# Kernel tuning notes

Measured on AMD Instinct MI355X. Metric: run time of the kernel, lower is better.

## Reference

```python
import jax, jax.numpy as jnp
import numpy as np

H, C = 2, 32  # heads, out_channels per head
NEG_SLOPE = 0.2


def gatv2_layer(h, src, dst, ea, W, b, We, att, bias, N):
    # shared lin_l = lin_r (share_weights=True)
    z = (h @ W + b).reshape(N, H, C)                      # [N,H,C]
    e = (ea @ We).reshape(-1, H, C)                        # [E',H,C]
    s = jax.nn.leaky_relu(z[dst] + z[src] + e, NEG_SLOPE)  # [E',H,C]
    alpha = jnp.einsum('ehc,hc->eh', s, att)               # [E',H]
    # segment softmax over destination neighborhoods
    m = jax.ops.segment_max(alpha, dst, num_segments=N)
    m = jnp.where(jnp.isfinite(m), m, 0.0)
    ex = jnp.exp(alpha - m[dst])
    denom = jax.ops.segment_sum(ex, dst, num_segments=N)
    a = ex / (denom[dst] + 1e-16)                          # [E',H]
    msg = (z[src] * a[:, :, None]).reshape(-1, H * C)      # [E',H*C]
    out = jax.ops.segment_sum(msg, dst, num_segments=N) + bias
    return out                                             # [N,H*C]


def setup_inputs() -> dict:
    key = jax.random.key(0)
    ks = jax.random.split(key, 16)
    N, E = 50000, 800000
    inp = {
        'x': jax.random.normal(ks[0], (N, 2), jnp.float32),
        'edge_index': jax.random.randint(ks[1], (2, E), 0, N, jnp.int64 if jax.config.jax_enable_x64 else jnp.int32).astype(jnp.int32),
        'edge_attr': jax.random.uniform(ks[2], (E, 2), jnp.float32),
        'dest_index': 123,
        'W0': jax.random.normal(ks[3], (2, 64), jnp.float32) * 0.5,
        'b0': jnp.zeros((64,), jnp.float32),
        'We0': jax.random.normal(ks[4], (2, 64), jnp.float32) * 0.5,
        'att0': jax.random.normal(ks[5], (H, C), jnp.float32) * 0.5,
        'bias0': jnp.zeros((64,), jnp.float32),
        'W1': jax.random.normal(ks[6], (64, 64), jnp.float32) * 0.125,
        'b1': jnp.zeros((64,), jnp.float32),
        'We1': jax.random.normal(ks[7], (2, 64), jnp.float32) * 0.5,
        'att1': jax.random.normal(ks[8], (H, C), jnp.float32) * 0.5,
        'bias1': jnp.zeros((64,), jnp.float32),
        'Wm1': jax.random.normal(ks[9], (194, 32), jnp.float32) * 0.07,
        'bm1': jnp.zeros((32,), jnp.float32),
        'Wm2': jax.random.normal(ks[10], (32, 1), jnp.float32) * 0.17,
        'bm2': jnp.zeros((1,), jnp.float32),
    }
    return inp


def reference(x, edge_index, edge_attr, dest_index,
              W0, b0, We0, att0, bias0,
              W1, b1, We1, att1, bias1,
              Wm1, bm1, Wm2, bm2):
    N = x.shape[0]
    # add self loops (fill_value='mean' for edge_attr)
    loops = jnp.arange(N, dtype=edge_index.dtype)
    src = jnp.concatenate([edge_index[0], loops])
    dst = jnp.concatenate([edge_index[1], loops])
    ea_sl = jnp.concatenate(
        [edge_attr, jnp.broadcast_to(edge_attr.mean(axis=0), (N, edge_attr.shape[1]))], axis=0)

    h = x
    h = jax.nn.elu(gatv2_layer(h, src, dst, ea_sl, W0, b0, We0, att0, bias0, N))
    h = jax.nn.elu(gatv2_layer(h, src, dst, ea_sl, W1, b1, We1, att1, bias1, N))

    goal = h[dest_index]                                   # [64]
    src_emb = h[edge_index[0]]                             # [E,64]
    dst_emb = h[edge_index[1]]                             # [E,64]
    goal_rep = jnp.broadcast_to(goal, (edge_index.shape[1], goal.shape[0]))
    edge_in = jnp.concatenate([src_emb, dst_emb, goal_rep, edge_attr], axis=-1)  # [E,194]
    hmlp = jax.nn.relu(edge_in @ Wm1 + bm1)
    logits = (hmlp @ Wm2 + bm2).squeeze(-1)                # [E]
    return logits
```

## Files before the change

### kernel.cpp

```cpp
#include <hip/hip_runtime.h>
#include <hip/hip_bf16.h>
#include <hip/hip_fp16.h>
#include <math.h>


typedef __attribute__((ext_vector_type(8))) short short8;
typedef __attribute__((ext_vector_type(4))) float f32x4;

#define BSH 7
#define CAP 4096
#define CH 4096

template <int IMM>
__device__ __forceinline__ float swz(float x) {
    return __int_as_float(__builtin_amdgcn_ds_swizzle(__float_as_int(x), IMM));
}

template <int CTRL>
__device__ __forceinline__ float dpp_add(float p) {
    int t = __builtin_amdgcn_update_dpp(0, __float_as_int(p), CTRL, 0xF, 0xF, true);
    return p + __int_as_float(t);
}

__device__ __forceinline__ short2 bsplit(float x) {
    unsigned u = __float_as_uint(x);
    short hi = (short)(u >> 16);
    float hif = __uint_as_float(u & 0xFFFF0000u);
    short lo = (short)(__float_as_uint(x - hif) >> 16);
    return make_short2(hi, lo);
}

__global__ __launch_bounds__(512) void setup_kernel(const float* __restrict__ W1,
                                                    const float* __restrict__ Wm1,
                                                    short* __restrict__ BfW1,
                                                    short* __restrict__ BfWm,
                                                    int* __restrict__ bucket_cursor,
                                                    float* __restrict__ easum, int nbuck) {
    if (blockIdx.x == 2) {
        for (int i = threadIdx.x; i < nbuck; i += 512) bucket_cursor[i] = i * CAP;
        if (threadIdx.x < 2) easum[threadIdx.x] = 0.f;
        return;
    }
    int snt = threadIdx.x >> 6;
    int lane = threadIdx.x & 63;
    int s = snt >> 2, nt = snt & 3;
    int col = nt * 16 + (lane & 15);
    short* Bf = blockIdx.x == 0 ? BfW1 : BfWm;
#pragma unroll
    for (int j = 0; j < 8; ++j) {
        int k = s * 32 + (lane >> 4) * 8 + j;
        float v;
        if (blockIdx.x == 0) {
            v = W1[k * 64 + col];
        } else {
            v = (col < 32) ? Wm1[k * 32 + col] : Wm1[(64 + k) * 32 + (col - 32)];
        }
        short2 t = bsplit(v);
        Bf[(snt * 2 + 0) * 512 + lane * 8 + j] = t.x;
        Bf[(snt * 2 + 1) * 512 + lane * 8 + j] = t.y;
    }
}

__global__ __launch_bounds__(256) void phaseA_kernel(const int* __restrict__ ei,
                                                     const float2* __restrict__ ea,
                                                     int* __restrict__ bucket_cursor,
                                                     float* __restrict__ easum,
                                                     float4* __restrict__ staged,
                                                     int E, int nbuck) {
    extern __shared__ int sm[];
    int* lcnt = sm;
    int* lbase = sm + nbuck;
    __shared__ float r0[4], r1[4];
    int tid = threadIdx.x;
    for (int i = tid; i < nbuck; i += 256) lcnt[i] = 0;
    __syncthreads();
    int base = blockIdx.x * CH;
    int end = min(base + CH, E);
    for (int i = base + tid; i < end; i += 256) {
        int d = ei[E + i];
        atomicAdd(&lcnt[d >> BSH], 1);
    }
    __syncthreads();
    for (int i = tid; i < nbuck; i += 256) {
        int c = lcnt[i];
        lbase[i] = c ? atomicAdd(&bucket_cursor[i], c) : 0;
        lcnt[i] = 0;
    }
    __syncthreads();
    float s0 = 0.f, s1 = 0.f;
    for (int i = base + tid; i < end; i += 256) {
        int s = ei[i], d = ei[E + i];
        float2 v = ea[i];
        s0 += v.x; s1 += v.y;
        int b = d >> BSH;
        int pos = lbase[b] + atomicAdd(&lcnt[b], 1);
        staged[pos] = make_float4(__int_as_float(s), v.x, v.y, __int_as_float(d));
    }
#pragma unroll
    for (int o = 32; o >= 1; o >>= 1) {
        s0 += __shfl_xor(s0, o);
        s1 += __shfl_xor(s1, o);
    }
    int wave = tid >> 6;
    if ((tid & 63) == 0) { r0[wave] = s0; r1[wave] = s1; }
    __syncthreads();
    if (tid == 0) {
        atomicAdd(&easum[0], r0[0] + r0[1] + r0[2] + r0[3]);
        atomicAdd(&easum[1], r1[0] + r1[1] + r1[2] + r1[3]);
    }
}

__global__ __launch_bounds__(512) void phaseB_mega(
    const float4* __restrict__ staged, const int* __restrict__ bucket_cursor,
    const float* __restrict__ easum, const float2* __restrict__ x,
    const float* __restrict__ W0, const float* __restrict__ b0,
    const float* __restrict__ We, const float* __restrict__ att,
    const float* __restrict__ bias, const short* __restrict__ Bf,
    const float* __restrict__ b1,
    int* __restrict__ row_ptr, float4* __restrict__ recs,
    __half* __restrict__ z16, int N, int E, int nbuck) {
    __shared__ int cnt128[128];
    __shared__ int offs[128];
    __shared__ int psum[512];
    __shared__ float acc6[128][6];
    __shared__ float h0s[128 * 64];
    int b = blockIdx.x;
    int n0g = b << BSH;
    int tid = threadIdx.x;
    int local = 0;
    for (int j = tid; j < b; j += 512) local += bucket_cursor[j] - j * CAP;
    psum[tid] = local;
    if (tid < 128) cnt128[tid] = 0;
    for (int i = tid; i < 128 * 6; i += 512) ((float*)acc6)[i] = 0.f;
    __syncthreads();
    for (int st = 256; st > 0; st >>= 1) {
        if (tid < st) psum[tid] += psum[tid + st];
        __syncthreads();
    }
    int bbase = psum[0] + 128 * b;
    int sbeg = b * CAP;
    int send = bucket_cursor[b];
    for (int i = sbeg + tid; i < send; i += 512) {
        int d = __float_as_int(staged[i].w);
        atomicAdd(&cnt128[d - n0g], 1);
    }
    __syncthreads();
    int node = n0g + tid;
    int tot = 0;
    if (tid < 128) {
        tot = cnt128[tid] + ((node < N) ? 1 : 0);
        offs[tid] = tot;
    }
    __syncthreads();
    for (int st = 1; st < 128; st <<= 1) {
        int v = 0;
        if (tid < 128) {
            v = offs[tid];
            if (tid >= st) v += offs[tid - st];
        }
        __syncthreads();
        if (tid < 128) offs[tid] = v;
        __syncthreads();
    }
    float invE = 1.f / (float)E;
    float m0 = easum[0] * invE, m1 = easum[1] * invE;
    if (tid < 128 && node < N) {
        int excl = bbase + offs[tid] - tot;
        row_ptr[node] = excl;
        recs[excl] = make_float4(__int_as_float(node), m0, m1, __int_as_float(node));
        offs[tid] = excl + 1;
    }
    int nodes_here = min(128, N - n0g);
    int nrec = (send - sbeg) + nodes_here;
    if (b == nbuck - 1 && tid == 0) row_ptr[N] = bbase + nrec;
    __syncthreads();
    for (int i = sbeg + tid; i < send; i += 512) {
        float4 r = staged[i];
        int d = __float_as_int(r.w);
        int pos = atomicAdd(&offs[d - n0g], 1);
        recs[pos] = r;
    }
    __syncthreads();

    int lane = tid & 63;
    int m = lane & 15, quad = lane >> 4;
    int wave = tid >> 6;
    {
        int c0 = quad * 8, c1 = 32 + c0;
        float w0a[8], w1a[8], ata[8], w0b[8], w1b[8], atb[8];
        float Wxa[8], Wya[8], bca[8], Wxb[8], Wyb[8], bcb[8];
#pragma unroll
        for (int j = 0; j < 8; ++j) {
            w0a[j] = We[c0 + j];  w1a[j] = We[64 + c0 + j];  ata[j] = att[c0 + j];
            w0b[j] = We[c1 + j];  w1b[j] = We[64 + c1 + j];  atb[j] = att[c1 + j];
            Wxa[j] = W0[c0 + j];  Wya[j] = W0[64 + c0 + j];  bca[j] = b0[c0 + j];
            Wxb[j] = W0[c1 + j];  Wyb[j] = W0[64 + c1 + j];  bcb[j] = b0[c1 + j];
        }
        int ntile = (nrec + 15) >> 4;
        int rend = bbase + nrec;
        for (int t = wave; t < ntile; t += 8) {
            int e = bbase + t * 16 + m;
            int ec = e < rend ? e : rend - 1;
            float4 r = recs[ec];
            int s = __float_as_int(r.x);
            int d = __float_as_int(r.w);
            float2 xs = x[s];
            float2 xd = x[d];
            float P0 = 0.f, P1 = 0.f;
#pragma unroll
            for (int j = 0; j < 8; ++j) {
                float zs = fmaf(xs.x, Wxa[j], fmaf(xs.y, Wya[j], bca[j]));
                float zd = fmaf(xd.x, Wxa[j], fmaf(xd.y, Wya[j], bca[j]));
                float t0 = zd + zs + fmaf(r.y, w0a[j], r.z * w1a[j]);
                t0 = fmaxf(t0, 0.2f * t0);
                P0 = fmaf(t0, ata[j], P0);
                float zs1 = fmaf(xs.x, Wxb[j], fmaf(xs.y, Wyb[j], bcb[j]));
                float zd1 = fmaf(xd.x, Wxb[j], fmaf(xd.y, Wyb[j], bcb[j]));
                float t1 = zd1 + zs1 + fmaf(r.y, w0b[j], r.z * w1b[j]);
                t1 = fmaxf(t1, 0.2f * t1);
                P1 = fmaf(t1, atb[j], P1);
            }
            P0 += swz<0x401F>(P0);
            P1 += swz<0x401F>(P1);
            P0 += __shfl_xor(P0, 32);
            P1 += __shfl_xor(P1, 32);
            float w0 = __expf(fminf(P0, 60.f));
            float w1 = __expf(fminf(P1, 60.f));
            if (lane < 16 && e < rend) {
                int dl = d - n0g;
                atomicAdd(&acc6[dl][0], w0);
                atomicAdd(&acc6[dl][1], w0 * xs.x);
                atomicAdd(&acc6[dl][2], w0 * xs.y);
                atomicAdd(&acc6[dl][3], w1);
                atomicAdd(&acc6[dl][4], w1 * xs.x);
                atomicAdd(&acc6[dl][5], w1 * xs.y);
            }
        }
    }
    __syncthreads();

    for (int idx = tid; idx < nodes_here * 64; idx += 512) {
        int q = idx >> 6;
        int ch = idx & 63;
        int hsel = (ch >= 32) ? 3 : 0;
        float l  = acc6[q][hsel];
        float Sx = acc6[q][hsel + 1];
        float Sy = acc6[q][hsel + 2];
        float num = fmaf(W0[ch], Sx, fmaf(W0[64 + ch], Sy, b0[ch] * l));
        float v = num / (l + 1e-16f) + bias[ch];
        v = (v > 0.f) ? v : expm1f(v);
        h0s[idx] = v;
    }
    for (int idx = nodes_here * 64 + tid; idx < 128 * 64; idx += 512) h0s[idx] = 0.f;
    __syncthreads();

    int rowb = wave * 16 + m;
    f32x4 acc[4] = {{0.f, 0.f, 0.f, 0.f}, {0.f, 0.f, 0.f, 0.f},
                    {0.f, 0.f, 0.f, 0.f}, {0.f, 0.f, 0.f, 0.f}};
#pragma unroll
    for (int s = 0; s < 2; ++s) {
        const float* ap = h0s + rowb * 64 + s * 32 + quad * 8;
        float4 a0 = *(const float4*)ap;
        float4 a1 = *(const float4*)(ap + 4);
        short8 ahi, alo;
        short2 t;
        t = bsplit(a0.x); ahi[0] = t.x; alo[0] = t.y;
        t = bsplit(a0.y); ahi[1] = t.x; alo[1] = t.y;
        t = bsplit(a0.z); ahi[2] = t.x; alo[2] = t.y;
        t = bsplit(a0.w); ahi[3] = t.x; alo[3] = t.y;
        t = bsplit(a1.x); ahi[4] = t.x; alo[4] = t.y;
        t = bsplit(a1.y); ahi[5] = t.x; alo[5] = t.y;
        t = bsplit(a1.z); ahi[6] = t.x; alo[6] = t.y;
        t = bsplit(a1.w); ahi[7] = t.x; alo[7] = t.y;
#pragma unroll
        for (int nt = 0; nt < 4; ++nt) {
            const short* bp = Bf + ((s * 4 + nt) * 2) * 512 + lane * 8;
            short8 bhi = *(const short8*)bp;
            short8 blo = *(const short8*)(bp + 512);
            acc[nt] = __builtin_amdgcn_mfma_f32_16x16x32_bf16(ahi, bhi, acc[nt], 0, 0, 0);
            acc[nt] = __builtin_amdgcn_mfma_f32_16x16x32_bf16(ahi, blo, acc[nt], 0, 0, 0);
            acc[nt] = __builtin_amdgcn_mfma_f32_16x16x32_bf16(alo, bhi, acc[nt], 0, 0, 0);
        }
    }
#pragma unroll
    for (int nt = 0; nt < 4; ++nt) {
        int col = nt * 16 + m;
        float bj = b1[col];
#pragma unroll
        for (int r = 0; r < 4; ++r) {
            int orow = n0g + wave * 16 + quad * 4 + r;
            if (orow < N) z16[(size_t)orow * 64 + col] = __float2half(acc[nt][r] + bj);
        }
    }
}

__global__ __launch_bounds__(256) void agg1_kernel(
    const __half* __restrict__ z, const int* __restrict__ row_ptr,
    const float4* __restrict__ recs,
    const float* __restrict__ We, const float* __restrict__ att,
    const float* __restrict__ bias, float* __restrict__ hout, int N) {
    int gtid = blockIdx.x * blockDim.x + threadIdx.x;
    int n = gtid >> 6;
    if (n >= N) return;
    n = __builtin_amdgcn_readfirstlane(n);
    int lane = threadIdx.x & 63;
    int half = lane >> 5;
    int c = (lane & 31) * 2;

    float We0a = We[c],      We0b = We[c + 1];
    float We1a = We[64 + c], We1b = We[64 + c + 1];
    float atta = att[c],     attb = att[c + 1];
    float2 znf = __half22float2(*(const __half2*)(z + (size_t)n * 64 + c));

    int beg = row_ptr[n], end = row_ptr[n + 1];
    float ll[4] = {0.f, 0.f, 0.f, 0.f};
    float a0[4] = {0.f, 0.f, 0.f, 0.f};
    float a1[4] = {0.f, 0.f, 0.f, 0.f};
    for (int i = beg; i < end; i += 8) {
        float w[4]; float2 zs[4];
#pragma unroll
        for (int k = 0; k < 4; ++k) {
            int idx = i + 2 * k + half;
            int idc = idx < end ? idx : end - 1;
            float4 r = recs[idc];
            int s = __float_as_int(r.x);
            zs[k] = __half22float2(*(const __half2*)(z + (size_t)s * 64 + c));
            float sj0 = znf.x + zs[k].x + fmaf(r.y, We0a, r.z * We1a);
            float sj1 = znf.y + zs[k].y + fmaf(r.y, We0b, r.z * We1b);
            sj0 = fmaxf(sj0, 0.2f * sj0);
            sj1 = fmaxf(sj1, 0.2f * sj1);
            float p = fmaf(sj0, atta, sj1 * attb);
            p = dpp_add<0xB1>(p);
            p = dpp_add<0x4E>(p);
            p = dpp_add<0x141>(p);
            p = dpp_add<0x140>(p);
            float ww = __expf(fminf(p, 60.f));
            w[k] = (idx < end) ? ww : 0.f;
        }
#pragma unroll
        for (int k = 0; k < 4; ++k) {
            ll[k] += w[k];
            a0[k] = fmaf(w[k], zs[k].x, a0[k]);
            a1[k] = fmaf(w[k], zs[k].y, a1[k]);
        }
    }
    float l  = (ll[0] + ll[1]) + (ll[2] + ll[3]);
    float s0 = (a0[0] + a0[1]) + (a0[2] + a0[3]);
    float s1 = (a1[0] + a1[1]) + (a1[2] + a1[3]);
    l  += __shfl_xor(l, 32);
    s0 += __shfl_xor(s0, 32);
    s1 += __shfl_xor(s1, 32);
    float inv = 1.f / (l + 1e-16f);
    float v0 = s0 * inv + bias[c];
    float v1 = s1 * inv + bias[c + 1];
    v0 = (v0 > 0.f) ? v0 : expm1f(v0);
    v1 = (v1 > 0.f) ? v1 : expm1f(v1);
    *(float2*)(hout + (size_t)n * 64 + c) = make_float2(v0, v1);
}

__global__ __launch_bounds__(256) void mfma_gemm64(const float* __restrict__ h,
                                                   const short* __restrict__ Bf,
                                                   __half* __restrict__ out, int N,
                                                   const float* __restrict__ Wm1,
                                                   const float* __restrict__ bm1,
                                                   const int* __restrict__ dest,
                                                   float* __restrict__ gv) {
    int wave = threadIdx.x >> 6;
    int lane = threadIdx.x & 63;
    int n0 = blockIdx.x * 64 + wave * 16;
    if (n0 < N) {
        int m = lane & 15, quad = lane >> 4;
        int arow = n0 + m;
        if (arow > N - 1) arow = N - 1;
        f32x4 acc[4] = {{0.f, 0.f, 0.f, 0.f}, {0.f, 0.f, 0.f, 0.f},
                        {0.f, 0.f, 0.f, 0.f}, {0.f, 0.f, 0.f, 0.f}};
#pragma unroll
        for (int s = 0; s < 2; ++s) {
            const float* ap = h + (size_t)arow * 64 + s * 32 + quad * 8;
            float4 a0 = *(const float4*)ap;
            float4 a1 = *(const float4*)(ap + 4);
            short8 ahi, alo;
            short2 t;
            t = bsplit(a0.x); ahi[0] = t.x; alo[0] = t.y;
            t = bsplit(a0.y); ahi[1] = t.x; alo[1] = t.y;
            t = bsplit(a0.z); ahi[2] = t.x; alo[2] = t.y;
            t = bsplit(a0.w); ahi[3] = t.x; alo[3] = t.y;
            t = bsplit(a1.x); ahi[4] = t.x; alo[4] = t.y;
            t = bsplit(a1.y); ahi[5] = t.x; alo[5] = t.y;
            t = bsplit(a1.z); ahi[6] = t.x; alo[6] = t.y;
            t = bsplit(a1.w); ahi[7] = t.x; alo[7] = t.y;
#pragma unroll
            for (int nt = 0; nt < 4; ++nt) {
                const short* bp = Bf + ((s * 4 + nt) * 2) * 512 + lane * 8;
                short8 bhi = *(const short8*)bp;
                short8 blo = *(const short8*)(bp + 512);
                acc[nt] = __builtin_amdgcn_mfma_f32_16x16x32_bf16(ahi, bhi, acc[nt], 0, 0, 0);
                acc[nt] = __builtin_amdgcn_mfma_f32_16x16x32_bf16(ahi, blo, acc[nt], 0, 0, 0);
                acc[nt] = __builtin_amdgcn_mfma_f32_16x16x32_bf16(alo, bhi, acc[nt], 0, 0, 0);
            }
        }
#pragma unroll
        for (int nt = 0; nt < 4; ++nt) {
            int col = nt * 16 + m;
#pragma unroll
            for (int r = 0; r < 4; ++r) {
                int orow = n0 + quad * 4 + r;
                if (orow < N) out[(size_t)orow * 64 + col] = __float2half(acc[nt][r]);
            }
        }
    }
    if (gv && blockIdx.x == 0 && threadIdx.x < 32) {
        int dd = dest[0];
        int q = threadIdx.x;
        float acc2 = bm1[q];
        for (int k = 0; k < 64; ++k)
            acc2 = fmaf(h[(size_t)dd * 64 + k], Wm1[(128 + k) * 32 + q], acc2);
        gv[q] = acc2;
    }
}

__global__ __launch_bounds__(256) void edge_mlp_kernel(
    const int* __restrict__ ei, const float2* __restrict__ ea,
    const __half* __restrict__ hsd, const float* __restrict__ gvec,
    const float* __restrict__ WrowA, const float* __restrict__ WrowB,
    const float* __restrict__ Wm2, const float* __restrict__ bm2,
    float* __restrict__ out, int E) {
    int tid = blockIdx.x * blockDim.x + threadIdx.x;
    int e = tid >> 3;
    int j = tid & 7;
    if (e >= E) return;
    int s = ei[e], d = ei[E + e];
    float2 eav = ea[e];
    const __half2* ps = (const __half2*)(hsd + (size_t)s * 64 + j * 4);
    const __half2* pd = (const __half2*)(hsd + (size_t)d * 64 + 32 + j * 4);
    float2 a01 = __half22float2(ps[0]), a23 = __half22float2(ps[1]);
    float2 b01 = __half22float2(pd[0]), b23 = __half22float2(pd[1]);
    float4 g = *(const float4*)(gvec + j * 4);
    float4 wa = *(const float4*)(WrowA + j * 4);
    float4 wb = *(const float4*)(WrowB + j * 4);
    float4 w2 = *(const float4*)(Wm2 + j * 4);
    float acc = 0.f, v;
    v = fmaf(eav.x, wa.x, fmaf(eav.y, wb.x, a01.x + b01.x + g.x)); v = fmaxf(v, 0.f); acc = fmaf(v, w2.x, acc);
    v = fmaf(eav.x, wa.y, fmaf(eav.y, wb.y, a01.y + b01.y + g.y)); v = fmaxf(v, 0.f); acc = fmaf(v, w2.y, acc);
    v = fmaf(eav.x, wa.z, fmaf(eav.y, wb.z, a23.x + b23.x + g.z)); v = fmaxf(v, 0.f); acc = fmaf(v, w2.z, acc);
    v = fmaf(eav.x, wa.w, fmaf(eav.y, wb.w, a23.y + b23.y + g.w)); v = fmaxf(v, 0.f); acc = fmaf(v, w2.w, acc);
    acc = dpp_add<0xB1>(acc);
    acc = dpp_add<0x4E>(acc);
    acc = dpp_add<0x141>(acc);
    if (j == 0) out[e] = acc + bm2[0];
}

extern "C" void kernel_launch(void* const* d_in, const int* in_sizes, int n_in,
                              void* d_out, int out_size, void* d_ws, size_t ws_size,
                              hipStream_t stream) {
    const float* x     = (const float*)d_in[0];
    const int*   ei    = (const int*)d_in[1];
    const float* ea    = (const float*)d_in[2];
    const int*   dest  = (const int*)d_in[3];
    const float* W0    = (const float*)d_in[4];
    const float* b0    = (const float*)d_in[5];
    const float* We0   = (const float*)d_in[6];
    const float* att0  = (const float*)d_in[7];
    const float* bias0 = (const float*)d_in[8];
    const float* W1    = (const float*)d_in[9];
    const float* b1    = (const float*)d_in[10];
    const float* We1   = (const float*)d_in[11];
    const float* att1  = (const float*)d_in[12];
    const float* bias1 = (const float*)d_in[13];
    const float* Wm1   = (const float*)d_in[14];
    const float* bm1   = (const float*)d_in[15];
    const float* Wm2   = (const float*)d_in[16];
    const float* bm2   = (const float*)d_in[17];

    const int N = in_sizes[0] / 2;
    const int E = in_sizes[1] / 2;
    const int nbuck = (N + 127) >> BSH;
    const int nchunk = (E + CH - 1) / CH;

    char* ws = (char*)d_ws;
    size_t off = 0;
    auto alloc = [&](size_t bytes) -> void* {
        void* p = ws + off;
        off += bytes;
        off = (off + 255) & ~(size_t)255;
        return p;
    };
    int*    bucket_cursor = (int*)alloc((size_t)nbuck * 4);
    int*    row_ptr       = (int*)alloc((size_t)(N + 1) * 4);
    size_t  slack_bytes   = (size_t)nbuck * CAP * 16;
    float4* staged        = (float4*)alloc(slack_bytes);
    float4* recs          = (float4*)alloc((size_t)(E + N) * 16);
    __half* z16           = (__half*)alloc((size_t)N * 64 * 2);
    float*  hbuf          = (float*)alloc((size_t)N * 64 * 4);
    float*  easum         = (float*)alloc(8);
    float*  gvec          = (float*)alloc(32 * 4);
    short*  BfW1          = (short*)alloc(8192 * 2);
    short*  BfWm          = (short*)alloc(8192 * 2);
    __half* hsd16         = z16;

    dim3 blk(256);
    setup_kernel<<<3, 512, 0, stream>>>(W1, Wm1, BfW1, BfWm, bucket_cursor, easum, nbuck);
    phaseA_kernel<<<nchunk, blk, (size_t)nbuck * 8, stream>>>(ei, (const float2*)ea,
                                                              bucket_cursor, easum,
                                                              staged, E, nbuck);
    phaseB_mega<<<nbuck, 512, 0, stream>>>(staged, bucket_cursor, easum,
                                           (const float2*)x, W0, b0, We0, att0, bias0,
                                           BfW1, b1, row_ptr, recs, z16, N, E, nbuck);
    agg1_kernel<<<(N * 64 + 255) / 256, blk, 0, stream>>>(z16, row_ptr, recs,
                                                          We1, att1, bias1, hbuf, N);
    mfma_gemm64<<<(N + 63) / 64, blk, 0, stream>>>(hbuf, BfWm, hsd16, N,
                                                   Wm1, bm1, dest, gvec);
    edge_mlp_kernel<<<((size_t)E * 8 + 255) / 256, blk, 0, stream>>>(
        ei, (const float2*)ea, hsd16, gvec,
        Wm1 + 192 * 32, Wm1 + 193 * 32, Wm2, bm2, (float*)d_out, E);
}
```

Baseline: 262.2 us.

## Halve node bucket size, interleave edge tiles and split MFMA columns across waves

Buckets shrink from 128 to 64 destination nodes (CAP halved), which doubles the number of phaseB blocks for more parallelism and cuts shared memory per block. The edge-scoring loop now gives each lane a strided edge index (m*ntile+t), so the 16 lanes of a tile touch different destinations and contend less on the shared-memory atomics. The dense 64x64 MFMA is split so that 8 waves cover 4 row tiles x 2 column halves. The risk is bucket overflow with CAP 2048 if a 64-node bucket receives more edges than it can stage, plus a longer prefix loop over twice as many buckets.

After: 256.9 us. -2.0%, faster.

```diff
diff --git a/kernel.cpp b/kernel.cpp
--- a/kernel.cpp
+++ b/kernel.cpp
@@ -7,8 +7,8 @@
 typedef __attribute__((ext_vector_type(8))) short short8;
 typedef __attribute__((ext_vector_type(4))) float f32x4;
 
-#define BSH 7
-#define CAP 4096
+#define BSH 6
+#define CAP 2048
 #define CH 4096
 
 template <int IMM>
@@ -119,58 +119,58 @@
     const float* __restrict__ b1,
     int* __restrict__ row_ptr, float4* __restrict__ recs,
     __half* __restrict__ z16, int N, int E, int nbuck) {
-    __shared__ int cnt128[128];
-    __shared__ int offs[128];
+    __shared__ int cnt64[64];
+    __shared__ int offs[64];
     __shared__ int psum[512];
-    __shared__ float acc6[128][6];
-    __shared__ float h0s[128 * 64];
+    __shared__ float acc6[64][6];
+    __shared__ float h0s[64 * 64];
     int b = blockIdx.x;
     int n0g = b << BSH;
     int tid = threadIdx.x;
     int local = 0;
     for (int j = tid; j < b; j += 512) local += bucket_cursor[j] - j * CAP;
     psum[tid] = local;
-    if (tid < 128) cnt128[tid] = 0;
-    for (int i = tid; i < 128 * 6; i += 512) ((float*)acc6)[i] = 0.f;
+    if (tid < 64) cnt64[tid] = 0;
+    for (int i = tid; i < 64 * 6; i += 512) ((float*)acc6)[i] = 0.f;
     __syncthreads();
     for (int st = 256; st > 0; st >>= 1) {
         if (tid < st) psum[tid] += psum[tid + st];
         __syncthreads();
     }
-    int bbase = psum[0] + 128 * b;
+    int bbase = psum[0] + 64 * b;
     int sbeg = b * CAP;
     int send = bucket_cursor[b];
     for (int i = sbeg + tid; i < send; i += 512) {
         int d = __float_as_int(staged[i].w);
-        atomicAdd(&cnt128[d - n0g], 1);
+        atomicAdd(&cnt64[d - n0g], 1);
     }
     __syncthreads();
     int node = n0g + tid;
     int tot = 0;
-    if (tid < 128) {
-        tot = cnt128[tid] + ((node < N) ? 1 : 0);
+    if (tid < 64) {
+        tot = cnt64[tid] + ((node < N) ? 1 : 0);
         offs[tid] = tot;
     }
     __syncthreads();
-    for (int st = 1; st < 128; st <<= 1) {
+    for (int st = 1; st < 64; st <<= 1) {
         int v = 0;
-        if (tid < 128) {
+        if (tid < 64) {
             v = offs[tid];
             if (tid >= st) v += offs[tid - st];
         }
         __syncthreads();
-        if (tid < 128) offs[tid] = v;
+        if (tid < 64) offs[tid] = v;
         __syncthreads();
     }
     float invE = 1.f / (float)E;
     float m0 = easum[0] * invE, m1 = easum[1] * invE;
-    if (tid < 128 && node < N) {
+    if (tid < 64 && node < N) {
         int excl = bbase + offs[tid] - tot;
         row_ptr[node] = excl;
         recs[excl] = make_float4(__int_as_float(node), m0, m1, __int_as_float(node));
         offs[tid] = excl + 1;
     }
-    int nodes_here = min(128, N - n0g);
+    int nodes_here = min(64, N - n0g);
     int nrec = (send - sbeg) + nodes_here;
     if (b == nbuck - 1 && tid == 0) row_ptr[N] = bbase + nrec;
     __syncthreads();
@@ -197,11 +197,11 @@
             Wxb[j] = W0[c1 + j];  Wyb[j] = W0[64 + c1 + j];  bcb[j] = b0[c1 + j];
         }
         int ntile = (nrec + 15) >> 4;
-        int rend = bbase + nrec;
         for (int t = wave; t < ntile; t += 8) {
-            int e = bbase + t * 16 + m;
-            int ec = e < rend ? e : rend - 1;
-            float4 r = recs[ec];
+            int el = m * ntile + t;
+            bool valid = el < nrec;
+            int e = bbase + (valid ? el : nrec - 1);
+            float4 r = recs[e];
             int s = __float_as_int(r.x);
             int d = __float_as_int(r.w);
             float2 xs = x[s];
@@ -226,7 +226,7 @@
             P1 += __shfl_xor(P1, 32);
             float w0 = __expf(fminf(P0, 60.f));
             float w1 = __expf(fminf(P1, 60.f));
-            if (lane < 16 && e < rend) {
+            if (lane < 16 && valid) {
                 int dl = d - n0g;
                 atomicAdd(&acc6[dl][0], w0);
                 atomicAdd(&acc6[dl][1], w0 * xs.x);
@@ -251,12 +251,12 @@
         v = (v > 0.f) ? v : expm1f(v);
         h0s[idx] = v;
     }
-    for (int idx = nodes_here * 64 + tid; idx < 128 * 64; idx += 512) h0s[idx] = 0.f;
-    __syncthreads();
-
-    int rowb = wave * 16 + m;
-    f32x4 acc[4] = {{0.f, 0.f, 0.f, 0.f}, {0.f, 0.f, 0.f, 0.f},
-                    {0.f, 0.f, 0.f, 0.f}, {0.f, 0.f, 0.f, 0.f}};
+    for (int idx = nodes_here * 64 + tid; idx < 64 * 64; idx += 512) h0s[idx] = 0.f;
+    __syncthreads();
+
+    int rowb = (wave & 3) * 16 + m;
+    int ntb = (wave >> 2) * 2;
+    f32x4 acc[2] = {{0.f, 0.f, 0.f, 0.f}, {0.f, 0.f, 0.f, 0.f}};
 #pragma unroll
     for (int s = 0; s < 2; ++s) {
         const float* ap = h0s + rowb * 64 + s * 32 + quad * 8;
@@ -273,23 +273,23 @@
         t = bsplit(a1.z); ahi[6] = t.x; alo[6] = t.y;
         t = bsplit(a1.w); ahi[7] = t.x; alo[7] = t.y;
 #pragma unroll
-        for (int nt = 0; nt < 4; ++nt) {
-            const short* bp = Bf + ((s * 4 + nt) * 2) * 512 + lane * 8;
+        for (int u = 0; u < 2; ++u) {
+            const short* bp = Bf + ((s * 4 + ntb + u) * 2) * 512 + lane * 8;
             short8 bhi = *(const short8*)bp;
             short8 blo = *(const short8*)(bp + 512);
-            acc[nt] = __builtin_amdgcn_mfma_f32_16x16x32_bf16(ahi, bhi, acc[nt], 0, 0, 0);
-            acc[nt] = __builtin_amdgcn_mfma_f32_16x16x32_bf16(ahi, blo, acc[nt], 0, 0, 0);
-            acc[nt] = __builtin_amdgcn_mfma_f32_16x16x32_bf16(alo, bhi, acc[nt], 0, 0, 0);
-        }
-    }
-#pragma unroll
-    for (int nt = 0; nt < 4; ++nt) {
-        int col = nt * 16 + m;
+            acc[u] = __builtin_amdgcn_mfma_f32_16x16x32_bf16(ahi, bhi, acc[u], 0, 0, 0);
+            acc[u] = __builtin_amdgcn_mfma_f32_16x16x32_bf16(ahi, blo, acc[u], 0, 0, 0);
+            acc[u] = __builtin_amdgcn_mfma_f32_16x16x32_bf16(alo, bhi, acc[u], 0, 0, 0);
+        }
+    }
+#pragma unroll
+    for (int u = 0; u < 2; ++u) {
+        int col = (ntb + u) * 16 + m;
         float bj = b1[col];
 #pragma unroll
         for (int r = 0; r < 4; ++r) {
-            int orow = n0g + wave * 16 + quad * 4 + r;
-            if (orow < N) z16[(size_t)orow * 64 + col] = __float2half(acc[nt][r] + bj);
+            int orow = n0g + (wave & 3) * 16 + quad * 4 + r;
+            if (orow < N) z16[(size_t)orow * 64 + col] = __float2half(acc[u][r] + bj);
         }
     }
 }
@@ -474,7 +474,7 @@
 
     const int N = in_sizes[0] / 2;
     const int E = in_sizes[1] / 2;
-    const int nbuck = (N + 127) >> BSH;
+    const int nbuck = (N + 63) >> BSH;
     const int nchunk = (E + CH - 1) / CH;
 
     char* ws = (char*)d_ws;
```
